# Optimization experiments

Hardware: AMD Instinct MI355X
Metric: run time of the kernel (lower is better)

The kernel has to match this reference:

```python
import jax, jax.numpy as jnp
import numpy as np

N, D, C = 100000, 384, 8


def setup_inputs() -> dict:
    key = jax.random.key(0)
    k1, k2, k3, k4 = jax.random.split(key, 4)
    Y = jax.random.normal(k1, (N, D), dtype=jnp.float32)
    O = jax.random.bernoulli(k2, 0.9, (N, D))  # observation mask
    # learned VB parameters (as held in the nn.Parameters of VBPCA)
    mbar = 0.1 * jax.random.normal(k3, (D,), dtype=jnp.float32)
    wbar = 0.1 * jax.random.normal(k4, (D, C), dtype=jnp.float32)
    Sigmaw = jnp.broadcast_to(jnp.eye(C, dtype=jnp.float32), (D, C, C))
    vy = jnp.float32(1.0)
    return {"Y": Y, "O": O, "mbar": mbar, "wbar": wbar, "Sigmaw": Sigmaw, "vy": vy}


def reference(Y, O, mbar, wbar, Sigmaw, vy):
    O_ = O.astype(Y.dtype)            # [N, D]
    Y = jnp.nan_to_num(Y)
    # per-channel rank-c outer product plus Sigmaw: baddbmm(Sigmaw, wbar[:,:,None], wbar[:,None,:])
    OwwSw = Sigmaw + wbar[:, :, None] * wbar[:, None, :]            # [D, C, C]
    # accumulate over observed channels: [N, D] @ [D, C*C] -> [N, C, C]
    A = (O_ @ OwwSw.reshape(D, C * C)).reshape(-1, C, C)
    Ic = jnp.eye(C, dtype=Y.dtype)
    Sigma_xn = vy * jnp.linalg.inv(vy * Ic[None] + A)               # [N, C, C]
    # xbarn = einsum('nlk,ni,ik,ni->nl', Sigma_xn/vy, O_, wbar, Y - mbar)
    t = O_ * (Y - mbar)                                             # [N, D]
    proj = t @ wbar                                                 # [N, C]
    xbarn = jnp.einsum('nlk,nk->nl', Sigma_xn / vy, proj)           # [N, C]
    return xbarn, Sigma_xn
```

## Files before the change

### kernel.cpp

```cpp
#include <hip/hip_runtime.h>

#define NN 100000
#define DD 384
#define CC 8
#define ROWS 64

typedef unsigned int uint;
typedef _Float16 half8 __attribute__((ext_vector_type(8)));
typedef float floatx4 __attribute__((ext_vector_type(4)));

__device__ __forceinline__ constexpr int TIDX(int i, int j) { return i * (i + 1) / 2 + j; }

__device__ __forceinline__ uint pkh2(float a, float b) {
  return __builtin_bit_cast(uint, __builtin_amdgcn_cvt_pkrtz(a, b));
}

__global__ __launch_bounds__(64) void vbpca_prep(
    const float* __restrict__ wbar, const float* __restrict__ Sigmaw,
    uint4* __restrict__ bfrag) {
  const int l = threadIdx.x;
  const int kt = blockIdx.x;
  const int kgrp = l >> 4;
#pragma unroll
  for (int ct = 0; ct < 3; ++ct) {
    const int col = ct * 16 + (l & 15);
    int ii = 0;
#pragma unroll
    for (int t = 0; t < 7; ++t) {
      if ((ii + 1) * (ii + 2) / 2 <= col && ii < 7) ++ii;
    }
    const int jj = col - ii * (ii + 1) / 2;
    float v[8];
#pragma unroll
    for (int j = 0; j < 8; ++j) {
      const int d = kt * 32 + kgrp * 8 + j;
      float val;
      if (col < 36) {
        val = Sigmaw[(size_t)d * 64 + ii * 8 + jj] + wbar[d * 8 + ii] * wbar[d * 8 + jj];
      } else if (col < 44) {
        val = wbar[d * 8 + (col - 36)];
      } else {
        val = 0.f;
      }
      v[j] = val;
    }
    uint4 u;
    u.x = pkh2(v[0], v[1]); u.y = pkh2(v[2], v[3]);
    u.z = pkh2(v[4], v[5]); u.w = pkh2(v[6], v[7]);
    bfrag[(kt * 3 + ct) * 64 + l] = u;
  }
}

__global__ __launch_bounds__(256, 5) void vbpca_main(
    const float* __restrict__ Y, const int* __restrict__ O,
    const uint4* __restrict__ bfrag, const float* __restrict__ mbar,
    const float* __restrict__ vyp, float* __restrict__ out) {
  __shared__ float smemf[6656];
  float* mbar_l = smemf;
  uint* tile_l = (uint*)(smemf + 384);
  float* scat_l = smemf + 384;
  float* sigst = smemf + 384;
  float* xbst = smemf + 384 + 4160;

  const int tid = threadIdx.x;
  const int l = tid & 63;
  const int w = tid >> 6;

  for (int i = tid; i < DD; i += 256) mbar_l[i] = mbar[i];

  const int lrow0 = tid >> 3;
  const int c4 = tid & 7;
  int rg0 = blockIdx.x * ROWS + lrow0;
  if (rg0 >= NN) rg0 = NN - 1;
  int rg1 = blockIdx.x * ROWS + lrow0 + 32;
  if (rg1 >= NN) rg1 = NN - 1;

  float4 yA0, yA1, yB0, yB1;
  int4 oA0, oA1, oB0, oB1;
#define ISSUE(S0y, S0o, S1y, S1o, KT)                                      \
  {                                                                        \
    const size_t off0 = (size_t)rg0 * DD + (KT) * 32 + c4 * 4;             \
    const size_t off1 = (size_t)rg1 * DD + (KT) * 32 + c4 * 4;             \
    S0y = *reinterpret_cast<const float4*>(Y + off0);                      \
    S0o = *reinterpret_cast<const int4*>(O + off0);                        \
    S1y = *reinterpret_cast<const float4*>(Y + off1);                      \
    S1o = *reinterpret_cast<const int4*>(O + off1);                        \
  }

#define PACK(S0y, S0o, S1y, S1o, KT, BUF)                                   \
  {                                                                         \
    const float4 mb = *reinterpret_cast<const float4*>(mbar_l + (KT)*32 + c4 * 4); \
    uint* tb = tile_l + (BUF)*2560;                                         \
    {                                                                       \
      const float f0 = (float)S0o.x, f1 = (float)S0o.y;                     \
      const float f2 = (float)S0o.z, f3 = (float)S0o.w;                     \
      uint* b0 = tb + (2 * lrow0) * 20 + c4 * 2;                            \
      b0[0] = pkh2(f0, f1); b0[1] = pkh2(f2, f3);                           \
      uint* b1 = tb + (2 * lrow0 + 1) * 20 + c4 * 2;                        \
      b1[0] = pkh2(f0 * (S0y.x - mb.x), f1 * (S0y.y - mb.y));               \
      b1[1] = pkh2(f2 * (S0y.z - mb.z), f3 * (S0y.w - mb.w));               \
    }                                                                       \
    {                                                                       \
      const float f0 = (float)S1o.x, f1 = (float)S1o.y;                     \
      const float f2 = (float)S1o.z, f3 = (float)S1o.w;                     \
      uint* b0 = tb + (2 * (lrow0 + 32)) * 20 + c4 * 2;                     \
      b0[0] = pkh2(f0, f1); b0[1] = pkh2(f2, f3);                           \
      uint* b1 = tb + (2 * (lrow0 + 32) + 1) * 20 + c4 * 2;                 \
      b1[0] = pkh2(f0 * (S1y.x - mb.x), f1 * (S1y.y - mb.y));               \
      b1[1] = pkh2(f2 * (S1y.z - mb.z), f3 * (S1y.w - mb.w));               \
    }                                                                       \
  }

  floatx4 acc[2][3];
#pragma unroll
  for (int i = 0; i < 2; ++i)
#pragma unroll
    for (int j = 0; j < 3; ++j) acc[i][j] = (floatx4){0.f, 0.f, 0.f, 0.f};

#define MFMA_PHASE(KT, BUF)                                                 \
  {                                                                         \
    const uint* tb = tile_l + (BUF)*2560;                                   \
    const half8 a0 = *reinterpret_cast<const half8*>(                       \
        tb + ((2 * w) * 16 + (l & 15)) * 20 + (l >> 4) * 4);                \
    const half8 a1 = *reinterpret_cast<const half8*>(                       \
        tb + ((2 * w + 1) * 16 + (l & 15)) * 20 + (l >> 4) * 4);            \
    const half8 b0 = __builtin_bit_cast(half8, bfrag[((KT)*3 + 0) * 64 + l]); \
    const half8 b1 = __builtin_bit_cast(half8, bfrag[((KT)*3 + 1) * 64 + l]); \
    const half8 b2 = __builtin_bit_cast(half8, bfrag[((KT)*3 + 2) * 64 + l]); \
    acc[0][0] = __builtin_amdgcn_mfma_f32_16x16x32_f16(a0, b0, acc[0][0], 0, 0, 0); \
    acc[0][1] = __builtin_amdgcn_mfma_f32_16x16x32_f16(a0, b1, acc[0][1], 0, 0, 0); \
    acc[0][2] = __builtin_amdgcn_mfma_f32_16x16x32_f16(a0, b2, acc[0][2], 0, 0, 0); \
    acc[1][0] = __builtin_amdgcn_mfma_f32_16x16x32_f16(a1, b0, acc[1][0], 0, 0, 0); \
    acc[1][1] = __builtin_amdgcn_mfma_f32_16x16x32_f16(a1, b1, acc[1][1], 0, 0, 0); \
    acc[1][2] = __builtin_amdgcn_mfma_f32_16x16x32_f16(a1, b2, acc[1][2], 0, 0, 0); \
  }

  ISSUE(yA0, oA0, yA1, oA1, 0);
  ISSUE(yB0, oB0, yB1, oB1, 1);
  __syncthreads();

#pragma unroll 1
  for (int kt = 0; kt < 12; kt += 2) {
    PACK(yA0, oA0, yA1, oA1, kt, 0);
    if (kt + 2 < 12) ISSUE(yA0, oA0, yA1, oA1, kt + 2);
    __syncthreads();
    MFMA_PHASE(kt, 0);
    PACK(yB0, oB0, yB1, oB1, kt + 1, 1);
    if (kt + 3 < 12) ISSUE(yB0, oB0, yB1, oB1, kt + 3);
    __syncthreads();
    MFMA_PHASE(kt + 1, 1);
  }
  __syncthreads();

#pragma unroll
  for (int rtl = 0; rtl < 2; ++rtl) {
    const int rt = 2 * w + rtl;
#pragma unroll
    for (int ct = 0; ct < 3; ++ct) {
#pragma unroll
      for (int reg = 0; reg < 4; ++reg) {
        scat_l[(rt * 16 + (l >> 4) * 4 + reg) * 49 + ct * 16 + (l & 15)] =
            acc[rtl][ct][reg];
      }
    }
  }
  __syncthreads();

  float a[36], pr[CC];
  if (tid < 64) {
#pragma unroll
    for (int k = 0; k < 36; ++k) a[k] = scat_l[(2 * tid) * 49 + k];
#pragma unroll
    for (int j = 0; j < CC; ++j) pr[j] = scat_l[(2 * tid + 1) * 49 + 36 + j];
  }
  __syncthreads();

  if (tid < 64) {
    const int row = tid;
    const float vy = *vyp;

    float L[36];
#pragma unroll
    for (int j = 0; j < CC; ++j) {
      float s = a[TIDX(j, j)] + vy;
#pragma unroll
      for (int k = 0; k < CC; ++k) {
        if (k < j) s -= L[TIDX(j, k)] * L[TIDX(j, k)];
      }
      const float dj = sqrtf(s);
      L[TIDX(j, j)] = dj;
      const float invdj = 1.0f / dj;
#pragma unroll
      for (int i = j + 1; i < CC; ++i) {
        float tt = a[TIDX(i, j)];
#pragma unroll
        for (int k = 0; k < CC; ++k) {
          if (k < j) tt -= L[TIDX(i, k)] * L[TIDX(j, k)];
        }
        L[TIDX(i, j)] = tt * invdj;
      }
    }

    float invd[CC];
#pragma unroll
    for (int i = 0; i < CC; ++i) invd[i] = 1.0f / L[TIDX(i, i)];
    float Li[36];
#pragma unroll
    for (int j = 0; j < CC; ++j) {
      Li[TIDX(j, j)] = invd[j];
#pragma unroll
      for (int i = j + 1; i < CC; ++i) {
        float s = 0.f;
#pragma unroll
        for (int k = 0; k < CC; ++k) {
          if (k >= j && k < i) s += L[TIDX(i, k)] * Li[TIDX(k, j)];
        }
        Li[TIDX(i, j)] = -s * invd[i];
      }
    }

    float sig[36];
#pragma unroll
    for (int i = 0; i < CC; ++i) {
#pragma unroll
      for (int j = 0; j <= i; ++j) {
        float s = 0.f;
#pragma unroll
        for (int k = 0; k < CC; ++k) {
          if (k >= i) s += Li[TIDX(k, i)] * Li[TIDX(k, j)];
        }
        sig[TIDX(i, j)] = vy * s;
      }
    }

    float uvec[CC];
#pragma unroll
    for (int i = 0; i < CC; ++i) {
      float s = 0.f;
#pragma unroll
      for (int j = 0; j < CC; ++j) {
        if (j <= i) s += Li[TIDX(i, j)] * pr[j];
      }
      uvec[i] = s;
    }
#pragma unroll
    for (int ll = 0; ll < CC; ++ll) {
      float s = 0.f;
#pragma unroll
      for (int i = 0; i < CC; ++i) {
        if (i >= ll) s += Li[TIDX(i, ll)] * uvec[i];
      }
      xbst[row * 9 + ll] = s;
    }
#pragma unroll
    for (int i = 0; i < CC; ++i) {
#pragma unroll
      for (int j = 0; j < CC; ++j) {
        sigst[row * 65 + i * 8 + j] = (j <= i) ? sig[TIDX(i, j)] : sig[TIDX(j, i)];
      }
    }
  }
  __syncthreads();

  const int valid = (NN - blockIdx.x * ROWS < ROWS) ? (NN - blockIdx.x * ROWS) : ROWS;
  float* __restrict__ sig_out = out + (size_t)NN * CC + (size_t)blockIdx.x * ROWS * 64;
  for (int f = tid; f < valid * 64; f += 256) {
    sig_out[f] = sigst[(f >> 6) * 65 + (f & 63)];
  }
  float* __restrict__ xb_out = out + (size_t)blockIdx.x * ROWS * CC;
  for (int f = tid; f < valid * 8; f += 256) {
    xb_out[f] = xbst[(f >> 3) * 9 + (f & 7)];
  }
}

extern "C" void kernel_launch(void* const* d_in, const int* in_sizes, int n_in,
                              void* d_out, int out_size, void* d_ws, size_t ws_size,
                              hipStream_t stream) {
  const float* Y = (const float*)d_in[0];
  const int* O = (const int*)d_in[1];
  const float* mbar = (const float*)d_in[2];
  const float* wbar = (const float*)d_in[3];
  const float* Sigmaw = (const float*)d_in[4];
  const float* vyp = (const float*)d_in[5];
  float* out = (float*)d_out;
  uint4* bfrag = (uint4*)d_ws;

  vbpca_prep<<<12, 64, 0, stream>>>(wbar, Sigmaw, bfrag);
  vbpca_main<<<(NN + ROWS - 1) / ROWS, 256, 0, stream>>>(Y, O, bfrag, mbar, vyp, out);
}
```

Baseline: 100.8 us.

## Give each wave its own row tile to remove block-wide barriers in main loop

```diff
diff --git a/kernel.cpp b/kernel.cpp
--- a/kernel.cpp
+++ b/kernel.cpp
@@ -4,6 +4,9 @@
 #define DD 384
 #define CC 8
 #define ROWS 64
+#define WROWS 16
+#define CROWS 8
+#define TSTR 200
 
 typedef unsigned int uint;
 typedef _Float16 half8 __attribute__((ext_vector_type(8)));
@@ -51,117 +54,125 @@
   }
 }
 
-__global__ __launch_bounds__(256, 5) void vbpca_main(
+__global__ __launch_bounds__(256, 3) void vbpca_main(
     const float* __restrict__ Y, const int* __restrict__ O,
     const uint4* __restrict__ bfrag, const float* __restrict__ mbar,
     const float* __restrict__ vyp, float* __restrict__ out) {
-  __shared__ float smemf[6656];
-  float* mbar_l = smemf;
-  uint* tile_l = (uint*)(smemf + 384);
-  float* scat_l = smemf + 384;
-  float* sigst = smemf + 384;
-  float* xbst = smemf + 384 + 4160;
+  __shared__ uint smem[13184];
+  float* mbar_l = (float*)smem;
+  uint* tile = smem + 384;
+  float* scat_l = (float*)(smem + 384);
+  float* sigst = (float*)(smem + 384);
+  float* xbst = (float*)(smem + 384) + 4160;
 
   const int tid = threadIdx.x;
+  const int wu = __builtin_amdgcn_readfirstlane((int)(tid >> 6));
   const int l = tid & 63;
-  const int w = tid >> 6;
 
   for (int i = tid; i < DD; i += 256) mbar_l[i] = mbar[i];
-
-  const int lrow0 = tid >> 3;
-  const int c4 = tid & 7;
-  int rg0 = blockIdx.x * ROWS + lrow0;
-  if (rg0 >= NN) rg0 = NN - 1;
-  int rg1 = blockIdx.x * ROWS + lrow0 + 32;
-  if (rg1 >= NN) rg1 = NN - 1;
-
-  float4 yA0, yA1, yB0, yB1;
-  int4 oA0, oA1, oB0, oB1;
-#define ISSUE(S0y, S0o, S1y, S1o, KT)                                      \
-  {                                                                        \
-    const size_t off0 = (size_t)rg0 * DD + (KT) * 32 + c4 * 4;             \
-    const size_t off1 = (size_t)rg1 * DD + (KT) * 32 + c4 * 4;             \
-    S0y = *reinterpret_cast<const float4*>(Y + off0);                      \
-    S0o = *reinterpret_cast<const int4*>(O + off0);                        \
-    S1y = *reinterpret_cast<const float4*>(Y + off1);                      \
-    S1o = *reinterpret_cast<const int4*>(O + off1);                        \
-  }
-
-#define PACK(S0y, S0o, S1y, S1o, KT, BUF)                                   \
+  __syncthreads();
+
+  uint* wtile = tile + wu * (16 * TSTR);
+  const int r0c0 = blockIdx.x * ROWS + wu * WROWS;
+  const int r0c1 = r0c0 + CROWS;
+
+  float4 yv[2][3];
+  int4 ov[2][3];
+
+#define LOADSTG(B, S, R0)                                                   \
   {                                                                         \
-    const float4 mb = *reinterpret_cast<const float4*>(mbar_l + (KT)*32 + c4 * 4); \
-    uint* tb = tile_l + (BUF)*2560;                                         \
-    {                                                                       \
-      const float f0 = (float)S0o.x, f1 = (float)S0o.y;                     \
-      const float f2 = (float)S0o.z, f3 = (float)S0o.w;                     \
-      uint* b0 = tb + (2 * lrow0) * 20 + c4 * 2;                            \
-      b0[0] = pkh2(f0, f1); b0[1] = pkh2(f2, f3);                           \
-      uint* b1 = tb + (2 * lrow0 + 1) * 20 + c4 * 2;                        \
-      b1[0] = pkh2(f0 * (S0y.x - mb.x), f1 * (S0y.y - mb.y));               \
-      b1[1] = pkh2(f2 * (S0y.z - mb.z), f3 * (S0y.w - mb.w));               \
+    _Pragma("unroll") for (int j = 0; j < 3; ++j) {                         \
+      const int f4 = (S)*192 + j * 64 + l;  \
+      const int i = f4 / 96;                                                \
+      const int c96 = f4 - i * 96;                                          \
+      int row = (R0) + i;                                                   \
+      row = row < NN ? row : NN - 1;                                        \
+      const size_t off = (size_t)row * 96 + c96;                            \
+      yv[B][j] = reinterpret_cast<const float4*>(Y)[off];                   \
+      ov[B][j] = reinterpret_cast<const int4*>(O)[off];                     \
     }                                                                       \
-    {                                                                       \
-      const float f0 = (float)S1o.x, f1 = (float)S1o.y;                     \
-      const float f2 = (float)S1o.z, f3 = (float)S1o.w;                     \
-      uint* b0 = tb + (2 * (lrow0 + 32)) * 20 + c4 * 2;                     \
-      b0[0] = pkh2(f0, f1); b0[1] = pkh2(f2, f3);                           \
-      uint* b1 = tb + (2 * (lrow0 + 32) + 1) * 20 + c4 * 2;                 \
-      b1[0] = pkh2(f0 * (S1y.x - mb.x), f1 * (S1y.y - mb.y));               \
-      b1[1] = pkh2(f2 * (S1y.z - mb.z), f3 * (S1y.w - mb.w));               \
+  }
+
+#define PACKSTG(B, S)                                                       \
+  {                                                                         \
+    _Pragma("unroll") for (int j = 0; j < 3; ++j) {                         \
+      const int f4 = (S)*192 + j * 64 + l;                                  \
+      const int i = f4 / 96;                                                \
+      const int c96 = f4 - i * 96;                                          \
+      const float4 mb = *reinterpret_cast<const float4*>(mbar_l + c96 * 4); \
+      const float4 y = yv[B][j];                                            \
+      const int4 o = ov[B][j];                                              \
+      const float f0 = (float)o.x, f1 = (float)o.y;                         \
+      const float f2 = (float)o.z, f3 = (float)o.w;                         \
+      uint* po = wtile + (2 * i) * TSTR + c96 * 2;                          \
+      *reinterpret_cast<uint2*>(po) = make_uint2(pkh2(f0, f1), pkh2(f2, f3)); \
+      uint* pt = wtile + (2 * i + 1) * TSTR + c96 * 2;                      \
+      *reinterpret_cast<uint2*>(pt) =                                       \
+          make_uint2(pkh2(f0 * (y.x - mb.x), f1 * (y.y - mb.y)),            \
+                     pkh2(f2 * (y.z - mb.z), f3 * (y.w - mb.w)));           \
     }                                                                       \
   }
 
-  floatx4 acc[2][3];
-#pragma unroll
-  for (int i = 0; i < 2; ++i)
-#pragma unroll
-    for (int j = 0; j < 3; ++j) acc[i][j] = (floatx4){0.f, 0.f, 0.f, 0.f};
-
-#define MFMA_PHASE(KT, BUF)                                                 \
+  floatx4 accA[3], accB[3];
+#pragma unroll
+  for (int j = 0; j < 3; ++j) {
+    accA[j] = (floatx4){0.f, 0.f, 0.f, 0.f};
+    accB[j] = (floatx4){0.f, 0.f, 0.f, 0.f};
+  }
+
+#define MFMA_LOOP(ACC)                                                      \
   {                                                                         \
-    const uint* tb = tile_l + (BUF)*2560;                                   \
-    const half8 a0 = *reinterpret_cast<const half8*>(                       \
-        tb + ((2 * w) * 16 + (l & 15)) * 20 + (l >> 4) * 4);                \
-    const half8 a1 = *reinterpret_cast<const half8*>(                       \
-        tb + ((2 * w + 1) * 16 + (l & 15)) * 20 + (l >> 4) * 4);            \
-    const half8 b0 = __builtin_bit_cast(half8, bfrag[((KT)*3 + 0) * 64 + l]); \
-    const half8 b1 = __builtin_bit_cast(half8, bfrag[((KT)*3 + 1) * 64 + l]); \
-    const half8 b2 = __builtin_bit_cast(half8, bfrag[((KT)*3 + 2) * 64 + l]); \
-    acc[0][0] = __builtin_amdgcn_mfma_f32_16x16x32_f16(a0, b0, acc[0][0], 0, 0, 0); \
-    acc[0][1] = __builtin_amdgcn_mfma_f32_16x16x32_f16(a0, b1, acc[0][1], 0, 0, 0); \
-    acc[0][2] = __builtin_amdgcn_mfma_f32_16x16x32_f16(a0, b2, acc[0][2], 0, 0, 0); \
-    acc[1][0] = __builtin_amdgcn_mfma_f32_16x16x32_f16(a1, b0, acc[1][0], 0, 0, 0); \
-    acc[1][1] = __builtin_amdgcn_mfma_f32_16x16x32_f16(a1, b1, acc[1][1], 0, 0, 0); \
-    acc[1][2] = __builtin_amdgcn_mfma_f32_16x16x32_f16(a1, b2, acc[1][2], 0, 0, 0); \
-  }
-
-  ISSUE(yA0, oA0, yA1, oA1, 0);
-  ISSUE(yB0, oB0, yB1, oB1, 1);
-  __syncthreads();
-
-#pragma unroll 1
-  for (int kt = 0; kt < 12; kt += 2) {
-    PACK(yA0, oA0, yA1, oA1, kt, 0);
-    if (kt + 2 < 12) ISSUE(yA0, oA0, yA1, oA1, kt + 2);
-    __syncthreads();
-    MFMA_PHASE(kt, 0);
-    PACK(yB0, oB0, yB1, oB1, kt + 1, 1);
-    if (kt + 3 < 12) ISSUE(yB0, oB0, yB1, oB1, kt + 3);
-    __syncthreads();
-    MFMA_PHASE(kt + 1, 1);
-  }
-  __syncthreads();
-
-#pragma unroll
-  for (int rtl = 0; rtl < 2; ++rtl) {
-    const int rt = 2 * w + rtl;
-#pragma unroll
-    for (int ct = 0; ct < 3; ++ct) {
-#pragma unroll
-      for (int reg = 0; reg < 4; ++reg) {
-        scat_l[(rt * 16 + (l >> 4) * 4 + reg) * 49 + ct * 16 + (l & 15)] =
-            acc[rtl][ct][reg];
-      }
+    uint4 bf0 = bfrag[0 * 64 + l];                                          \
+    uint4 bf1 = bfrag[1 * 64 + l];                                          \
+    uint4 bf2 = bfrag[2 * 64 + l];                                          \
+    _Pragma("unroll") for (int kt = 0; kt < 12; ++kt) {                     \
+      const half8 av = *reinterpret_cast<const half8*>(                     \
+          wtile + (l & 15) * TSTR + kt * 16 + (l >> 4) * 4);                \
+      uint4 nb0, nb1, nb2;                                                  \
+      if (kt < 11) {                                                        \
+        nb0 = bfrag[((kt + 1) * 3 + 0) * 64 + l];                           \
+        nb1 = bfrag[((kt + 1) * 3 + 1) * 64 + l];                           \
+        nb2 = bfrag[((kt + 1) * 3 + 2) * 64 + l];                           \
+      }                                                                     \
+      ACC[0] = __builtin_amdgcn_mfma_f32_16x16x32_f16(                      \
+          av, __builtin_bit_cast(half8, bf0), ACC[0], 0, 0, 0);             \
+      ACC[1] = __builtin_amdgcn_mfma_f32_16x16x32_f16(                      \
+          av, __builtin_bit_cast(half8, bf1), ACC[1], 0, 0, 0);             \
+      ACC[2] = __builtin_amdgcn_mfma_f32_16x16x32_f16(                      \
+          av, __builtin_bit_cast(half8, bf2), ACC[2], 0, 0, 0);             \
+      bf0 = nb0; bf1 = nb1; bf2 = nb2;                                      \
+    }                                                                       \
+  }
+
+  LOADSTG(0, 0, r0c0);
+  LOADSTG(1, 1, r0c0);
+  PACKSTG(0, 0);
+  LOADSTG(0, 2, r0c0);
+  PACKSTG(1, 1);
+  LOADSTG(1, 3, r0c0);
+  PACKSTG(0, 2);
+  PACKSTG(1, 3);
+  LOADSTG(0, 0, r0c1);
+  LOADSTG(1, 1, r0c1);
+  MFMA_LOOP(accA);
+
+  PACKSTG(0, 0);
+  LOADSTG(0, 2, r0c1);
+  PACKSTG(1, 1);
+  LOADSTG(1, 3, r0c1);
+  PACKSTG(0, 2);
+  PACKSTG(1, 3);
+  MFMA_LOOP(accB);
+
+  __syncthreads();
+
+#pragma unroll
+  for (int ct = 0; ct < 3; ++ct) {
+#pragma unroll
+    for (int reg = 0; reg < 4; ++reg) {
+      const int m = (l >> 4) * 4 + reg;
+      scat_l[(wu * 32 + m) * 49 + ct * 16 + (l & 15)] = accA[ct][reg];
+      scat_l[(wu * 32 + 16 + m) * 49 + ct * 16 + (l & 15)] = accB[ct][reg];
     }
   }
   __syncthreads();
```

Measured after the change: 82.36 us. 18.3% less time.
